# Performance work log

Hardware: AMD Instinct MI355X
Metric: run time of the kernel (lower is better)

Reference implementation:

```python
import jax, jax.numpy as jnp
import numpy as np

THETA_ALPHA = 8.0
THETA_BETA = 3.0
DOWNSAMPLE = 4


def _make_w1():
    # spatial Gaussian kernel, cropped to the range-kernel radius
    r1 = int(THETA_ALPHA * 4)
    x, y = np.mgrid[-r1:r1 + 1, -r1:r1 + 1]
    w1 = np.exp(-(x ** 2 + y ** 2) / (2 * THETA_ALPHA ** 2))
    radius = int(THETA_BETA * 4)
    w1 = w1[r1 - radius:radius - r1, r1 - radius:radius - r1]  # [25, 25]
    return jnp.asarray(w1, dtype=jnp.float32), radius


def _extract_patches(x, radius, mode):
    # x: [B, H, W, C] -> [B, H, W, ps, ps, C] via gather from padded array
    ps = 2 * radius + 1
    pad = [(0, 0), (radius, radius), (radius, radius), (0, 0)]
    xp = jnp.pad(x, pad, mode=mode)
    B, H, W, C = x.shape
    I = jnp.arange(H)[:, None] + jnp.arange(ps)[None, :]  # [H, ps]
    J = jnp.arange(W)[:, None] + jnp.arange(ps)[None, :]  # [W, ps]
    return xp[:, I[:, None, :, None], J[None, :, None, :], :]


def setup_inputs() -> dict:
    key = jax.random.key(0)
    k1, k2 = jax.random.split(key)
    src = jax.random.normal(k1, (1, 512, 512, 21), dtype=jnp.float32)
    im = jax.random.uniform(k2, (1, 512, 512, 3), dtype=jnp.float32)
    return {"src": src, "im": im}


def reference(src, im):
    w1, radius = _make_w1()
    B, H, W, Cs = src.shape
    rH, rW = H // DOWNSAMPLE, W // DOWNSAMPLE
    src_r = jax.image.resize(src, (B, rH, rW, Cs), method='bilinear')
    im_r = jax.image.resize(im, (B, rH, rW, im.shape[-1]), method='bilinear')

    # range kernel from guide image patches
    w = _extract_patches(im_r, radius, 'reflect')  # [B,rH,rW,ps,ps,Ci]
    w = w - im_r[:, :, :, None, None, :]
    w = jnp.sum(w ** 2, axis=-1, keepdims=True)  # [B,rH,rW,ps,ps,1]
    w = jnp.exp(-w / (2 * THETA_BETA ** 2))
    w = w * w1[None, None, None, :, :, None]

    # weighted neighborhood sum of src (zero-padded)
    p = _extract_patches(src_r, radius, 'constant')  # [B,rH,rW,ps,ps,Cs]
    out = jnp.sum(p * w, axis=(3, 4))  # [B,rH,rW,Cs]
    return jax.image.resize(out, (B, H, W, Cs), method='bilinear')
```

## Files before the change

### kernel.cpp

```cpp
#include <hip/hip_runtime.h>
#include <hip/hip_fp16.h>

#define RH 128
#define RW 128
#define CS 21
#define IH 512
#define IW 512
#define NPIX (RH * RW)
#define P 5
#define SPITCH 160
#define SCH8 (RH * SPITCH)
#define IPITCH 152
#define STW 88

#define NB_H (((IH / 4) * RW * CS + 255) / 256)
__global__ void fused_ds_kernel(const float* __restrict__ src, const float* __restrict__ im,
                                __half* __restrict__ tmpH, float2* __restrict__ imh) {
    if (blockIdx.x < NB_H) {
        int idx = blockIdx.x * 256 + threadIdx.x;
        if (idx >= (IH / 4) * RW * CS) return;
        int c = idx % CS;
        int t = idx / CS;
        int x = t % RW;
        int y4 = t / RW;
        int y0 = y4 * 4;

        float sx = 4.f * x + 1.5f;
        float wx[8]; int jx[8]; float wxs = 0.f;
#pragma unroll
        for (int k = 0; k < 8; ++k) {
            int j = 4 * x - 2 + k;
            float w = 1.f - fabsf(sx - (float)j) * 0.25f;
            if (j < 0 || j >= IW) { w = 0.f; j = 0; }
            jx[k] = j; wx[k] = w; wxs += w;
        }
        float inv = 1.f / wxs;
#pragma unroll
        for (int r = 0; r < 4; ++r) {
            const float* row = src + (size_t)(y0 + r) * IW * CS + c;
            float s = 0.f;
#pragma unroll
            for (int b = 0; b < 8; ++b) s += wx[b] * row[jx[b] * CS];
            tmpH[((size_t)(y0 + r) * RW + x) * CS + c] = __float2half(s * inv);
        }
    } else {
        int idx = (blockIdx.x - NB_H) * 256 + threadIdx.x;
        if (idx >= RH * IPITCH) return;
        int xp = idx % IPITCH;
        int y = idx / IPITCH;
        int gx = xp - 12;
        gx = gx < 0 ? -gx : (gx > RW - 1 ? 2 * (RW - 1) - gx : gx);

        float wy[8], wx[8];
        int jy[8], jx[8];
        float sy = 4.f * y + 1.5f, sx = 4.f * gx + 1.5f;
        float wys = 0.f, wxs = 0.f;
#pragma unroll
        for (int k = 0; k < 8; ++k) {
            int j = 4 * y - 2 + k;
            float w = 1.f - fabsf(sy - (float)j) * 0.25f;
            if (j < 0 || j >= IH) { w = 0.f; j = 0; }
            jy[k] = j; wy[k] = w; wys += w;
            int j2 = 4 * gx - 2 + k;
            float w2 = 1.f - fabsf(sx - (float)j2) * 0.25f;
            if (j2 < 0 || j2 >= IW) { w2 = 0.f; j2 = 0; }
            jx[k] = j2; wx[k] = w2; wxs += w2;
        }
        float inv = 1.f / (wys * wxs);
        float s0 = 0.f, s1 = 0.f, s2 = 0.f;
#pragma unroll
        for (int a = 0; a < 8; ++a) {
            const float* row = im + (size_t)(jy[a] * IW) * 3;
            float r0 = 0.f, r1 = 0.f, r2 = 0.f;
#pragma unroll
            for (int b = 0; b < 8; ++b) {
                const float* pp = row + jx[b] * 3;
                r0 += wx[b] * pp[0];
                r1 += wx[b] * pp[1];
                r2 += wx[b] * pp[2];
            }
            s0 += wy[a] * r0; s1 += wy[a] * r1; s2 += wy[a] * r2;
        }
        float2 o;
        *reinterpret_cast<__half2*>(&o.x) = __floats2half2_rn(s0 * inv, s1 * inv);
        *reinterpret_cast<__half2*>(&o.y) = __floats2half2_rn(s2 * inv, 0.f);
        imh[idx] = o;
    }
}

__global__ void ds_src_v_kernel(const __half* __restrict__ tmpH, __half* __restrict__ srcP) {
    int idx = blockIdx.x * blockDim.x + threadIdx.x;
    if (idx >= RH * SPITCH * 24) return;
    int c = idx % 24;
    int t = idx / 24;
    int xp = t % SPITCH;
    int y = t / SPITCH;
    int g = c >> 3;
    size_t oidx = ((size_t)(g * RH + y) * SPITCH + xp) * 8 + (c & 7);
    int x = xp - 12;
    if (c >= CS || x < 0 || x >= RW) { srcP[oidx] = __float2half(0.f); return; }

    float sy = 4.f * y + 1.5f;
    float wy[8]; int jy[8]; float wys = 0.f;
#pragma unroll
    for (int k = 0; k < 8; ++k) {
        int j = 4 * y - 2 + k;
        float w = 1.f - fabsf(sy - (float)j) * 0.25f;
        if (j < 0 || j >= IH) { w = 0.f; j = 0; }
        jy[k] = j; wy[k] = w; wys += w;
    }
    float s = 0.f;
#pragma unroll
    for (int a = 0; a < 8; ++a)
        s += wy[a] * __half2float(tmpH[((size_t)jy[a] * RW + x) * CS + c]);
    srcP[oidx] = __float2half(s / wys);
}

__global__ __launch_bounds__(256) void bilateral_kernel(
        const float4* __restrict__ srcP8,
        const float2* __restrict__ imh,
        __half* __restrict__ part) {
    __shared__ float4 sst[5][3][STW];

    int tid = threadIdx.x;
    int w = tid >> 6;
    int lane = tid & 63;
    int bid = blockIdx.x;
    int p = bid >> 8;
    int pxw = bid & 255;
    int h = pxw & 1;
    int y = pxw >> 1;
    int xbase = h << 6;
    int x = xbase + lane;

    for (int t = tid; t < 5 * 3 * STW; t += 256) {
        int r = t / (3 * STW);
        int rem = t - r * (3 * STW);
        int g = rem / STW;
        int i = rem - g * STW;
        int ry = y + p + 5 * r - 12;
        float4 v = {0.f, 0.f, 0.f, 0.f};
        if (ry >= 0 && ry < RH)
            v = srcP8[(size_t)(g * RH + ry) * SPITCH + xbase + i];
        sst[r][g][i] = v;
    }
    __syncthreads();

    float2 craw = imh[y * IPITCH + x + 12];
    __half2 ch01 = *reinterpret_cast<__half2*>(&craw.x);
    __half2 ch23 = *reinterpret_cast<__half2*>(&craw.y);
    float2 f01 = __half22float2(ch01);
    float c0 = f01.x, c1 = f01.y, c2 = __half2float(__low2half(ch23));

    float4 a0 = {0,0,0,0}, a1 = {0,0,0,0}, a2 = {0,0,0,0},
           a3 = {0,0,0,0}, a4 = {0,0,0,0}, a5 = {0,0,0,0};

    for (int r = 0; r < 5; ++r) {
        int dy = p + 5 * r;
        int ry = y + dy - 12;
        int ryc = min(max(ry, 0), RH - 1);
        float fdy = (float)(dy - 12);
        float gy = fdy * fdy;
        const float2* irow = imh + ryc * IPITCH + x;

        float cwv[7];
#pragma unroll
        for (int i = 0; i < 7; ++i) {
            int dx = w + 4 * i;
            int dxc = min(dx, 24);
            float2 raw = irow[dxc];
            __half2 h01 = *reinterpret_cast<__half2*>(&raw.x);
            __half2 h23 = *reinterpret_cast<__half2*>(&raw.y);
            float2 rg = __half22float2(h01);
            float d0 = rg.x - c0;
            float d1 = rg.y - c1;
            float d2 = __half2float(__low2half(h23)) - c2;
            float fdx = (float)(dx - 12);
            float e = -(d0 * d0 + d1 * d1 + d2 * d2) * (1.f / 18.f)
                      - (gy + fdx * fdx) * (1.f / 128.f);
            cwv[i] = (dx < 25) ? __expf(e) : 0.f;
        }

        __half2 hacc[12];
#pragma unroll
        for (int k = 0; k < 12; ++k) hacc[k] = __floats2half2_rn(0.f, 0.f);

#pragma unroll
        for (int i = 0; i < 7; ++i) {
            int dxc = min(w + 4 * i, 24);
            __half2 cw2 = __float2half2_rn(cwv[i]);
            float4 s0 = sst[r][0][lane + dxc];
            float4 s1 = sst[r][1][lane + dxc];
            float4 s2 = sst[r][2][lane + dxc];
            const __half2* h0 = reinterpret_cast<const __half2*>(&s0);
            const __half2* h1 = reinterpret_cast<const __half2*>(&s1);
            const __half2* h2 = reinterpret_cast<const __half2*>(&s2);
#pragma unroll
            for (int k = 0; k < 4; ++k) {
                hacc[k]     = __hfma2(cw2, h0[k], hacc[k]);
                hacc[4 + k] = __hfma2(cw2, h1[k], hacc[4 + k]);
                hacc[8 + k] = __hfma2(cw2, h2[k], hacc[8 + k]);
            }
        }
        float2 u;
        u = __half22float2(hacc[0]);  a0.x += u.x; a0.y += u.y;
        u = __half22float2(hacc[1]);  a0.z += u.x; a0.w += u.y;
        u = __half22float2(hacc[2]);  a1.x += u.x; a1.y += u.y;
        u = __half22float2(hacc[3]);  a1.z += u.x; a1.w += u.y;
        u = __half22float2(hacc[4]);  a2.x += u.x; a2.y += u.y;
        u = __half22float2(hacc[5]);  a2.z += u.x; a2.w += u.y;
        u = __half22float2(hacc[6]);  a3.x += u.x; a3.y += u.y;
        u = __half22float2(hacc[7]);  a3.z += u.x; a3.w += u.y;
        u = __half22float2(hacc[8]);  a4.x += u.x; a4.y += u.y;
        u = __half22float2(hacc[9]);  a4.z += u.x; a4.w += u.y;
        u = __half22float2(hacc[10]); a5.x += u.x; a5.y += u.y;
        u = __half22float2(hacc[11]); a5.z += u.x; a5.w += u.y;
    }

    __syncthreads();
    float4* redp = &sst[0][0][0];
    if (w > 0) {
        int base = (w - 1) * 6 * 64 + lane;
        redp[base + 0 * 64] = a0; redp[base + 1 * 64] = a1; redp[base + 2 * 64] = a2;
        redp[base + 3 * 64] = a3; redp[base + 4 * 64] = a4; redp[base + 5 * 64] = a5;
    }
    __syncthreads();
    if (w == 0) {
        float4 b[6] = {a0, a1, a2, a3, a4, a5};
#pragma unroll
        for (int k = 0; k < 6; ++k) {
#pragma unroll
            for (int r = 0; r < 3; ++r) {
                float4 v = redp[(r * 6 + k) * 64 + lane];
                b[k].x += v.x; b[k].y += v.y; b[k].z += v.z; b[k].w += v.w;
            }
        }
        int pix = (y << 7) + x;
        __half* po = part + ((size_t)(p * CS) << 14) + pix;
#pragma unroll
        for (int c = 0; c < CS; ++c) {
            float v = (&b[c >> 2].x)[c & 3];
            po[(size_t)c << 14] = __float2half(v);
        }
    }
}

__global__ void reduce_kernel(const __half* __restrict__ part, float* __restrict__ outr24) {
    int t = blockIdx.x * blockDim.x + threadIdx.x;
    if (t >= CS * (NPIX / 4)) return;
    int c = t >> 12;
    int i4 = t & 4095;
    int pix0 = i4 << 2;
    float4 s = {0, 0, 0, 0};
#pragma unroll
    for (int p = 0; p < P; ++p) {
        const __half* pp = part + ((size_t)(p * CS + c) << 14) + pix0;
        __half2 v01 = *reinterpret_cast<const __half2*>(pp);
        __half2 v23 = *reinterpret_cast<const __half2*>(pp + 2);
        float2 f01 = __half22float2(v01);
        float2 f23 = __half22float2(v23);
        s.x += f01.x; s.y += f01.y; s.z += f23.x; s.w += f23.y;
    }
    outr24[(size_t)(pix0 + 0) * 24 + c] = s.x;
    outr24[(size_t)(pix0 + 1) * 24 + c] = s.y;
    outr24[(size_t)(pix0 + 2) * 24 + c] = s.z;
    outr24[(size_t)(pix0 + 3) * 24 + c] = s.w;
}

__global__ void upsample_kernel(const float4* __restrict__ inr24, float* __restrict__ out) {
    int idx = blockIdx.x * blockDim.x + threadIdx.x;
    if (idx >= IH * IW * 6) return;
    int g = idx % 6;
    int t = idx / 6;
    int X = t % IW, Y = t / IW;
    float fy = 0.25f * (float)Y - 0.375f;
    float fx = 0.25f * (float)X - 0.375f;
    int y0 = (int)floorf(fy); float ty = fy - (float)y0;
    int x0 = (int)floorf(fx); float tx = fx - (float)x0;
    int y1 = y0 + 1, x1 = x0 + 1;
    y0 = min(max(y0, 0), RH - 1); y1 = min(max(y1, 0), RH - 1);
    x0 = min(max(x0, 0), RW - 1); x1 = min(max(x1, 0), RW - 1);
    float4 v00 = inr24[((y0 << 7) + x0) * 6 + g], v01 = inr24[((y0 << 7) + x1) * 6 + g];
    float4 v10 = inr24[((y1 << 7) + x0) * 6 + g], v11 = inr24[((y1 << 7) + x1) * 6 + g];
    float4 v0, v1, r;
    v0.x = v00.x + tx * (v01.x - v00.x); v1.x = v10.x + tx * (v11.x - v10.x);
    v0.y = v00.y + tx * (v01.y - v00.y); v1.y = v10.y + tx * (v11.y - v10.y);
    v0.z = v00.z + tx * (v01.z - v00.z); v1.z = v10.z + tx * (v11.z - v10.z);
    v0.w = v00.w + tx * (v01.w - v00.w); v1.w = v10.w + tx * (v11.w - v10.w);
    r.x = v0.x + ty * (v1.x - v0.x);
    r.y = v0.y + ty * (v1.y - v0.y);
    r.z = v0.z + ty * (v1.z - v0.z);
    r.w = v0.w + ty * (v1.w - v0.w);
    float* o = out + (size_t)(Y * IW + X) * CS + 4 * g;
    if (g < 5) { o[0] = r.x; o[1] = r.y; o[2] = r.z; o[3] = r.w; }
    else       { o[0] = r.x; }
}

extern "C" void kernel_launch(void* const* d_in, const int* in_sizes, int n_in,
                              void* d_out, int out_size, void* d_ws, size_t ws_size,
                              hipStream_t stream) {
    const float* src = (const float*)d_in[0];
    const float* im  = (const float*)d_in[1];
    float* out = (float*)d_out;
    char* ws = (char*)d_ws;

    __half* tmpH = (__half*)d_out;
    __half* part = (__half*)d_out;
    __half* srcP = (__half*)((char*)d_out + 21037056);
    float2* imh  = (float2*)ws;
    float* out_r24 = (float*)(ws + 155648);

    int nb_im = (RH * IPITCH + 255) / 256;
    fused_ds_kernel<<<NB_H + nb_im, 256, 0, stream>>>(src, im, tmpH, imh);

    int tv = RH * SPITCH * 24;
    ds_src_v_kernel<<<(tv + 255) / 256, 256, 0, stream>>>(tmpH, srcP);

    bilateral_kernel<<<P * 256, 256, 0, stream>>>((const float4*)srcP, imh, part);

    int tr = CS * (NPIX / 4);
    reduce_kernel<<<(tr + 255) / 256, 256, 0, stream>>>(part, out_r24);

    int t3 = IH * IW * 6;
    upsample_kernel<<<(t3 + 255) / 256, 256, 0, stream>>>((const float4*)out_r24, out);
}
```

Before: 56.98 us.

## Fuse partial-sum reduction into bilateral kernel via last-block atomic counter

Removes the separate reduce kernel launch. Each bilateral block increments a per-tile atomic counter, and the fifth (last) block to finish reduces the five half-precision partial sums for that tile and writes outr24. Counters are zeroed in the first downsample kernel. This saves a launch and its tail, but adds threadfences, an atomic per block and serialized reduction work in the last-arriving blocks.

```diff
diff --git a/kernel.cpp b/kernel.cpp
--- a/kernel.cpp
+++ b/kernel.cpp
@@ -15,7 +15,9 @@
 
 #define NB_H (((IH / 4) * RW * CS + 255) / 256)
 __global__ void fused_ds_kernel(const float* __restrict__ src, const float* __restrict__ im,
-                                __half* __restrict__ tmpH, float2* __restrict__ imh) {
+                                __half* __restrict__ tmpH, float2* __restrict__ imh,
+                                unsigned* __restrict__ counters) {
+    if (blockIdx.x == 0) counters[threadIdx.x] = 0;
     if (blockIdx.x < NB_H) {
         int idx = blockIdx.x * 256 + threadIdx.x;
         if (idx >= (IH / 4) * RW * CS) return;
@@ -119,8 +121,11 @@
 __global__ __launch_bounds__(256) void bilateral_kernel(
         const float4* __restrict__ srcP8,
         const float2* __restrict__ imh,
-        __half* __restrict__ part) {
+        __half* __restrict__ part,
+        float* __restrict__ outr24,
+        unsigned* __restrict__ counters) {
     __shared__ float4 sst[5][3][STW];
+    __shared__ int lastFlag;
 
     int tid = threadIdx.x;
     int w = tid >> 6;
@@ -243,28 +248,37 @@
             po[(size_t)c << 14] = __float2half(v);
         }
     }
-}
-
-__global__ void reduce_kernel(const __half* __restrict__ part, float* __restrict__ outr24) {
-    int t = blockIdx.x * blockDim.x + threadIdx.x;
-    if (t >= CS * (NPIX / 4)) return;
-    int c = t >> 12;
-    int i4 = t & 4095;
-    int pix0 = i4 << 2;
-    float4 s = {0, 0, 0, 0};
-#pragma unroll
-    for (int p = 0; p < P; ++p) {
-        const __half* pp = part + ((size_t)(p * CS + c) << 14) + pix0;
-        __half2 v01 = *reinterpret_cast<const __half2*>(pp);
-        __half2 v23 = *reinterpret_cast<const __half2*>(pp + 2);
-        float2 f01 = __half22float2(v01);
-        float2 f23 = __half22float2(v23);
-        s.x += f01.x; s.y += f01.y; s.z += f23.x; s.w += f23.y;
-    }
-    outr24[(size_t)(pix0 + 0) * 24 + c] = s.x;
-    outr24[(size_t)(pix0 + 1) * 24 + c] = s.y;
-    outr24[(size_t)(pix0 + 2) * 24 + c] = s.z;
-    outr24[(size_t)(pix0 + 3) * 24 + c] = s.w;
+
+    __syncthreads();
+    if (tid == 0) {
+        __threadfence();
+        unsigned old = atomicAdd(&counters[pxw], 1u);
+        lastFlag = (old == 4u);
+    }
+    __syncthreads();
+    if (lastFlag) {
+        __threadfence();
+        int q0 = ((y << 7) + xbase) >> 2;
+        for (int t2 = tid; t2 < CS * 16; t2 += 256) {
+            int c = t2 >> 4;
+            int q = t2 & 15;
+            int pix0 = (q0 + q) << 2;
+            float4 s = {0, 0, 0, 0};
+#pragma unroll
+            for (int pp = 0; pp < P; ++pp) {
+                const __half* pb = part + ((size_t)(pp * CS + c) << 14) + pix0;
+                __half2 v01 = *reinterpret_cast<const __half2*>(pb);
+                __half2 v23 = *reinterpret_cast<const __half2*>(pb + 2);
+                float2 g01 = __half22float2(v01);
+                float2 g23 = __half22float2(v23);
+                s.x += g01.x; s.y += g01.y; s.z += g23.x; s.w += g23.y;
+            }
+            outr24[(size_t)(pix0 + 0) * 24 + c] = s.x;
+            outr24[(size_t)(pix0 + 1) * 24 + c] = s.y;
+            outr24[(size_t)(pix0 + 2) * 24 + c] = s.z;
+            outr24[(size_t)(pix0 + 3) * 24 + c] = s.w;
+        }
+    }
 }
 
 __global__ void upsample_kernel(const float4* __restrict__ inr24, float* __restrict__ out) {
@@ -309,17 +323,15 @@
     __half* srcP = (__half*)((char*)d_out + 21037056);
     float2* imh  = (float2*)ws;
     float* out_r24 = (float*)(ws + 155648);
+    unsigned* counters = (unsigned*)(ws + 1728512);
 
     int nb_im = (RH * IPITCH + 255) / 256;
-    fused_ds_kernel<<<NB_H + nb_im, 256, 0, stream>>>(src, im, tmpH, imh);
+    fused_ds_kernel<<<NB_H + nb_im, 256, 0, stream>>>(src, im, tmpH, imh, counters);
 
     int tv = RH * SPITCH * 24;
     ds_src_v_kernel<<<(tv + 255) / 256, 256, 0, stream>>>(tmpH, srcP);
 
-    bilateral_kernel<<<P * 256, 256, 0, stream>>>((const float4*)srcP, imh, part);
-
-    int tr = CS * (NPIX / 4);
-    reduce_kernel<<<(tr + 255) / 256, 256, 0, stream>>>(part, out_r24);
+    bilateral_kernel<<<P * 256, 256, 0, stream>>>((const float4*)srcP, imh, part, out_r24, counters);
 
     int t3 = IH * IW * 6;
     upsample_kernel<<<(t3 + 255) / 256, 256, 0, stream>>>((const float4*)out_r24, out);
```

Result: slower. 104.1 us (+82.7%).

## Fuse partial-sum reduction with bilinear upsample into one tiled kernel

Applied to the files above, without the earlier changes.

Adds a reduce_up kernel in which each block reduces the five half-precision partial sums for a 6x6 low-res halo into shared memory, then bilinearly upsamples a 16x16 output tile straight to the output. This removes one launch and the global round trip of the intermediate low-res float buffer. Because the partials can no longer live in the output buffer, they move to the workspace and the guide buffer moves into d_out, all gated on workspace size, with the old path kept as a fallback. Halo reads overlap between neighbouring blocks, so some partial data is read more than once.

```diff
diff --git a/kernel.cpp b/kernel.cpp
--- a/kernel.cpp
+++ b/kernel.cpp
@@ -12,6 +12,7 @@
 #define SCH8 (RH * SPITCH)
 #define IPITCH 152
 #define STW 88
+#define UT 16
 
 #define NB_H (((IH / 4) * RW * CS + 255) / 256)
 __global__ void fused_ds_kernel(const float* __restrict__ src, const float* __restrict__ im,
@@ -242,6 +243,73 @@
             float v = (&b[c >> 2].x)[c & 3];
             po[(size_t)c << 14] = __float2half(v);
         }
+    }
+}
+
+__global__ __launch_bounds__(256) void reduce_up_kernel(const __half* __restrict__ part,
+                                                        float* __restrict__ out) {
+    __shared__ float red[6][6][24];
+    int tid = threadIdx.x;
+    int b = blockIdx.x;
+    int X0 = (b & 31) << 4;
+    int Y0 = (b >> 5) << 4;
+    int ry0 = (Y0 >> 2) - 1;
+    int rx0 = (X0 >> 2) - 1;
+
+    for (int t = tid; t < 36 * CS; t += 256) {
+        int c = t / 36;
+        int rem = t - c * 36;
+        int py = rem / 6, px = rem - (rem / 6) * 6;
+        int gy = min(max(ry0 + py, 0), RH - 1);
+        int gx = min(max(rx0 + px, 0), RW - 1);
+        int pix = (gy << 7) + gx;
+        float s = 0.f;
+#pragma unroll
+        for (int p = 0; p < P; ++p)
+            s += __half2float(part[((size_t)(p * CS + c) << 14) + pix]);
+        red[py][px][c] = s;
+    }
+    for (int t = tid; t < 36 * 3; t += 256) {
+        int c = 21 + t / 36;
+        int rem = t % 36;
+        red[rem / 6][rem % 6][c] = 0.f;
+    }
+    __syncthreads();
+
+    for (int t = tid; t < UT * UT * 6; t += 256) {
+        int g = t % 6;
+        int t2 = t / 6;
+        int xloc = t2 % UT;
+        int yloc = t2 / UT;
+        int X = X0 + xloc, Y = Y0 + yloc;
+        float fy = 0.25f * (float)Y - 0.375f;
+        float fx = 0.25f * (float)X - 0.375f;
+        int y0 = (int)floorf(fy); float ty = fy - (float)y0;
+        int x0 = (int)floorf(fx); float tx = fx - (float)x0;
+        int j0 = min(max(y0, 0), RH - 1) - ry0;
+        int j1 = min(max(y0 + 1, 0), RH - 1) - ry0;
+        int i0 = min(max(x0, 0), RW - 1) - rx0;
+        int i1 = min(max(x0 + 1, 0), RW - 1) - rx0;
+        const float* p00 = &red[j0][i0][4 * g];
+        const float* p01 = &red[j0][i1][4 * g];
+        const float* p10 = &red[j1][i0][4 * g];
+        const float* p11 = &red[j1][i1][4 * g];
+        float4 v00 = *reinterpret_cast<const float4*>(p00);
+        float4 v01 = *reinterpret_cast<const float4*>(p01);
+        float4 v10 = *reinterpret_cast<const float4*>(p10);
+        float4 v11 = *reinterpret_cast<const float4*>(p11);
+        float4 v0, v1, r;
+        v0.x = v00.x + tx * (v01.x - v00.x); v1.x = v10.x + tx * (v11.x - v10.x);
+        v0.y = v00.y + tx * (v01.y - v00.y); v1.y = v10.y + tx * (v11.y - v10.y);
+        v0.z = v00.z + tx * (v01.z - v00.z); v1.z = v10.z + tx * (v11.z - v10.z);
+        v0.w = v00.w + tx * (v01.w - v00.w); v1.w = v10.w + tx * (v11.w - v10.w);
+        r.x = v0.x + ty * (v1.x - v0.x);
+        r.y = v0.y + ty * (v1.y - v0.y);
+        r.z = v0.z + ty * (v1.z - v0.z);
+        r.w = v0.w + ty * (v1.w - v0.w);
+        float* o = out + (size_t)(Y * IW + X) * CS + 4 * g;
+        if (g < 5) { o[0] = r.x; o[1] = r.y; o[2] = r.z; o[3] = r.w; }
+        else       { o[0] = r.x; }
     }
 }
 
@@ -304,23 +372,42 @@
     float* out = (float*)d_out;
     char* ws = (char*)d_ws;
 
+    const size_t PART_BYTES = (size_t)P * CS * NPIX * 2;
+    bool merged = ws_size >= PART_BYTES;
+
     __half* tmpH = (__half*)d_out;
-    __half* part = (__half*)d_out;
     __half* srcP = (__half*)((char*)d_out + 21037056);
-    float2* imh  = (float2*)ws;
-    float* out_r24 = (float*)(ws + 155648);
-
-    int nb_im = (RH * IPITCH + 255) / 256;
-    fused_ds_kernel<<<NB_H + nb_im, 256, 0, stream>>>(src, im, tmpH, imh);
-
-    int tv = RH * SPITCH * 24;
-    ds_src_v_kernel<<<(tv + 255) / 256, 256, 0, stream>>>(tmpH, srcP);
-
-    bilateral_kernel<<<P * 256, 256, 0, stream>>>((const float4*)srcP, imh, part);
-
-    int tr = CS * (NPIX / 4);
-    reduce_kernel<<<(tr + 255) / 256, 256, 0, stream>>>(part, out_r24);
-
-    int t3 = IH * IW * 6;
-    upsample_kernel<<<(t3 + 255) / 256, 256, 0, stream>>>((const float4*)out_r24, out);
-}
+
+    if (merged) {
+        __half* part = (__half*)ws;
+        float2* imh  = (float2*)((char*)d_out + 16777216);
+
+        int nb_im = (RH * IPITCH + 255) / 256;
+        fused_ds_kernel<<<NB_H + nb_im, 256, 0, stream>>>(src, im, tmpH, imh);
+
+        int tv = RH * SPITCH * 24;
+        ds_src_v_kernel<<<(tv + 255) / 256, 256, 0, stream>>>(tmpH, srcP);
+
+        bilateral_kernel<<<P * 256, 256, 0, stream>>>((const float4*)srcP, imh, part);
+
+        reduce_up_kernel<<<(IW / UT) * (IH / UT), 256, 0, stream>>>(part, out);
+    } else {
+        __half* part = (__half*)d_out;
+        float2* imh  = (float2*)ws;
+        float* out_r24 = (float*)(ws + 155648);
+
+        int nb_im = (RH * IPITCH + 255) / 256;
+        fused_ds_kernel<<<NB_H + nb_im, 256, 0, stream>>>(src, im, tmpH, imh);
+
+        int tv = RH * SPITCH * 24;
+        ds_src_v_kernel<<<(tv + 255) / 256, 256, 0, stream>>>(tmpH, srcP);
+
+        bilateral_kernel<<<P * 256, 256, 0, stream>>>((const float4*)srcP, imh, part);
+
+        int tr = CS * (NPIX / 4);
+        reduce_kernel<<<(tr + 255) / 256, 256, 0, stream>>>(part, out_r24);
+
+        int t3 = IH * IW * 6;
+        upsample_kernel<<<(t3 + 255) / 256, 256, 0, stream>>>((const float4*)out_r24, out);
+    }
+}
```

Result: faster. 52.25 us, median of 2 (-8.3%).
